# Kernel tuning notes

Hardware: AMD Instinct MI355X
Metric: run time of the kernel (lower is better)

## Reference

```python
import jax, jax.numpy as jnp
import numpy as np

N_PTS = 20000  # points per cloud


def setup_inputs() -> dict:
    key = jax.random.key(0)
    k1, k2 = jax.random.split(key)
    preds = jax.random.normal(k1, (N_PTS, 3), dtype=jnp.float32)
    gts = jax.random.normal(k2, (1, N_PTS, 3), dtype=jnp.float32)
    return {"preds": preds, "gts": gts}


def reference(preds, gts):
    # x = gts: [B, Nx, 3]; y = preds.unsqueeze(0): [1, Ny, 3] (B must be 1 for bmm)
    y = preds[None]                                   # [1, Ny, 3]
    x = gts                                           # [1, Nx, 3]
    xx = jnp.sum(x * x, axis=-1)                      # [1, Nx]  (diag of x x^T)
    yy = jnp.sum(y * y, axis=-1)                      # [1, Ny]
    zz = jnp.einsum('bnd,bmd->bnm', x, y)             # [1, Nx, Ny]
    P = xx[:, :, None] + yy[:, None, :] - 2.0 * zz    # [1, Nx, Ny] squared dists
    dist1 = jnp.min(P, axis=1)                        # [1, Ny] min over gts points
    dist2 = jnp.min(P, axis=2)                        # [1, Nx] min over pred points
    idx1 = jnp.argmin(P, axis=1)                      # [1, Ny]
    idx2 = jnp.argmin(P, axis=2)                      # [1, Nx]
    return dist1, dist2, idx1, idx2
```

## Files before the change

### kernel.cpp

```cpp
#include <hip/hip_runtime.h>

#define N_PTS  20000
#define NG     128
#define NC     (NG * NG)
#define GMIN   (-6.0f)
#define GINV   (NG / 12.0f)
#define MARGIN 5e-4f
#define SSTRIDE (N_PTS / 64)
#define QB79   79

__device__ __forceinline__ float np_self_dot(float x, float y, float z) {
    return __fadd_rn(__fadd_rn(__fmul_rn(x, x), __fmul_rn(y, y)),
                     __fmul_rn(z, z));
}
__device__ __forceinline__ unsigned ordmap(float f) {
    unsigned b = __float_as_uint(f);
    return (b & 0x80000000u) ? ~b : (b | 0x80000000u);
}
__device__ __forceinline__ float invord(unsigned h) {
    return __uint_as_float((h & 0x80000000u) ? (h ^ 0x80000000u) : ~h);
}
__device__ __forceinline__ int cellC(float v) {
    int c = (int)((v - GMIN) * GINV);
    return c < 0 ? 0 : (c > NG - 1 ? NG - 1 : c);
}
__device__ __forceinline__ unsigned long long wave_min_u64(unsigned long long k) {
    #pragma unroll
    for (int m = 1; m < 64; m <<= 1) {
        unsigned long long o = __shfl_xor(k, m, 64);
        k = (o < k) ? o : k;
    }
    return k;
}
__device__ __forceinline__ int imin2(int a, int b) { return a < b ? a : b; }
__device__ __forceinline__ int imax2(int a, int b) { return a > b ? a : b; }

#define EVAL2(r)                                                           \
    {   float rx = (r).x, ry = (r).y, rz = (r).z;                          \
        float sr = np_self_dot(rx, ry, rz);                                \
        unsigned ridx = __float_as_uint((r).w);                            \
        float za = __fadd_rn(__fadd_rn(__fmul_rn(qax, rx),                 \
                                       __fmul_rn(qay, ry)),                \
                             __fmul_rn(qaz, rz));                          \
        float Pa = __fsub_rn(__fadd_rn(sqa, sr), __fadd_rn(za, za));       \
        unsigned long long kka =                                           \
            ((unsigned long long)ordmap(Pa) << 32) | ridx;                 \
        ka = (kka < ka) ? kka : ka;                                        \
        float zb = __fadd_rn(__fadd_rn(__fmul_rn(qbx, rx),                 \
                                       __fmul_rn(qby, ry)),                \
                             __fmul_rn(qbz, rz));                          \
        float Pb = __fsub_rn(__fadd_rn(sqb, sr), __fadd_rn(zb, zb));       \
        unsigned long long kkb =                                           \
            ((unsigned long long)ordmap(Pb) << 32) | ridx;                 \
        kb = (kkb < kb) ? kkb : kb; }

__global__ __launch_bounds__(256) void k_hist(
    const float* __restrict__ preds, const float* __restrict__ gts,
    int* __restrict__ cursor)
{
    int t = blockIdx.x * 256 + threadIdx.x;
    if (t >= 2 * N_PTS) return;
    int cl = t / N_PTS, i = t - cl * N_PTS;
    const float* src = cl ? gts : preds;
    int cell = cellC(src[i*3+0]) * NG + cellC(src[i*3+1]);
    atomicAdd(&cursor[cl * NC + cell], 1);
}

__global__ __launch_bounds__(1024) void k_scan(
    int* __restrict__ cursor, int* __restrict__ bstart)
{
    __shared__ int wsum[16];
    __shared__ int wpre[16];
    int cl = blockIdx.x, t = threadIdx.x;
    int wave = t >> 6, lane = t & 63;

    int base = cl * NC + t * 16;
    const int4* c4 = (const int4*)(cursor + base);
    int4 a = c4[0], b = c4[1], c = c4[2], d = c4[3];
    int v[16] = { a.x, a.y, a.z, a.w, b.x, b.y, b.z, b.w,
                  c.x, c.y, c.z, c.w, d.x, d.y, d.z, d.w };
    int s = 0;
    #pragma unroll
    for (int i = 0; i < 16; ++i) s += v[i];

    int ps = s;
    #pragma unroll
    for (int m = 1; m < 64; m <<= 1) {
        int o = __shfl_up(ps, m, 64);
        if (lane >= m) ps += o;
    }
    if (lane == 63) wsum[wave] = ps;
    __syncthreads();
    if (t < 16) {
        int x = wsum[t];
        int px = x;
        #pragma unroll
        for (int m = 1; m < 16; m <<= 1) {
            int o = __shfl_up(px, m, 16);
            if ((t & 15) >= m) px += o;
        }
        wpre[t] = px - x;
    }
    __syncthreads();

    int run = wpre[wave] + (ps - s);
    #pragma unroll
    for (int i = 0; i < 16; ++i) {
        bstart[cl * (NC + 1) + t * 16 + i] = run;
        cursor[base + i] = run;
        run += v[i];
    }
    if (t == 1023) bstart[cl * (NC + 1) + NC] = run;
}

__global__ __launch_bounds__(256) void k_scatter(
    const float* __restrict__ preds, const float* __restrict__ gts,
    int* __restrict__ cursor, float4* __restrict__ sorted)
{
    int t = blockIdx.x * 256 + threadIdx.x;
    if (t >= 2 * N_PTS) return;
    int cl = t / N_PTS, i = t - cl * N_PTS;
    const float* src = cl ? gts : preds;
    float x = src[i*3+0], y = src[i*3+1], z = src[i*3+2];
    int cell = cellC(x) * NG + cellC(y);
    int pos = atomicAdd(&cursor[cl * NC + cell], 1);
    sorted[(size_t)cl * N_PTS + pos] = make_float4(x, y, z, __int_as_float(i));
}

__global__ __launch_bounds__(64) void k_main(
    const float4* __restrict__ sorted, const int* __restrict__ bstart,
    float* __restrict__ out)
{
    int wid  = blockIdx.x;
    int lane = threadIdx.x;
    int q0   = wid * 2;
    int dir  = q0 / N_PTS;
    int qp0  = q0 - dir * N_PTS;
    int rcl  = 1 - dir;

    const float4* rs = sorted + (size_t)rcl * N_PTS;
    const int*    cs = bstart + rcl * (NC + 1);

    float4 samp = rs[lane * SSTRIDE];
    float4 qva  = sorted[(size_t)dir * N_PTS + qp0];
    float4 qvb  = sorted[(size_t)dir * N_PTS + qp0 + 1];
    int oa = __float_as_int(qva.w), ob = __float_as_int(qvb.w);
    float qax = qva.x, qay = qva.y, qaz = qva.z;
    float qbx = qvb.x, qby = qvb.y, qbz = qvb.z;
    float sqa = np_self_dot(qax, qay, qaz);
    float sqb = np_self_dot(qbx, qby, qbz);

    unsigned long long ka = ~0ULL, kb = ~0ULL;
    int l31 = lane & 31;

#define SCAN_RECT(xL, xR, yL, yR)                                          \
    {   int R = (xR) - (xL) + 1;                                           \
        for (int g = 0; g < R; g += 32) {                                  \
            int rows = R - g; if (rows > 32) rows = 32;                    \
            int xr  = (xL) + g + (l31 < rows ? l31 : rows - 1);            \
            int col = (lane < 32) ? (yL) : ((yR) + 1);                     \
            int b2 = cs[xr * NG + col];                                    \
            for (int r0 = 0; r0 < rows; r0 += 3) {                         \
                int i1 = r0 + 1 < rows ? r0 + 1 : rows - 1;                \
                int i2 = r0 + 2 < rows ? r0 + 2 : rows - 1;                \
                int L0 = __shfl(b2, r0, 64), H0 = __shfl(b2, 32 + r0, 64); \
                int L1 = __shfl(b2, i1, 64), H1 = __shfl(b2, 32 + i1, 64); \
                int L2 = __shfl(b2, i2, 64), H2 = __shfl(b2, 32 + i2, 64); \
                int d0 = H0 - L0;                                          \
                int d1 = (r0 + 1 < rows) ? H1 - L1 : 0;                    \
                int d2 = (r0 + 2 < rows) ? H2 - L2 : 0;                    \
                int s01 = d0 + d1, tot = s01 + d2;                         \
                int t = lane;                                              \
                if (t < tot) {                                             \
                    int p = t < d0 ? L0 + t : t < s01 ? L1 + (t - d0)      \
                                                      : L2 + (t - s01);   \
                    float4 rc = rs[p];                                     \
                    for (t += 64; t < tot; t += 64) {                      \
                        int pn = t < d0 ? L0 + t : t < s01 ? L1 + (t - d0) \
                                                           : L2 + (t - s01);\
                        float4 rn = rs[pn];                                \
                        EVAL2(rc)                                          \
                        rc = rn;                                           \
                    }                                                      \
                    EVAL2(rc)                                              \
                }                                                          \
            }                                                              \
        }                                                                  \
    }

    int cxa = cellC(qax), cya = cellC(qay);
    int cxb = cellC(qbx), cyb = cellC(qby);
    int sxL = imax2(imin2(cxa, cxb) - 1, 0);
    int sxR = imin2(imax2(cxa, cxb) + 1, NG - 1);
    int syL = imax2(imin2(cya, cyb) - 1, 0);
    int syR = imin2(imax2(cya, cyb) + 1, NG - 1);
    SCAN_RECT(sxL, sxR, syL, syR)
    EVAL2(samp)

    ka = wave_min_u64(ka);
    kb = wave_min_u64(kb);
    float Wa = sqrtf(invord((unsigned)(ka >> 32)) + MARGIN);
    float Wb = sqrtf(invord((unsigned)(kb >> 32)) + MARGIN);
    int txL = imin2(cellC(qax - Wa), cellC(qbx - Wb));
    int txR = imax2(cellC(qax + Wa), cellC(qbx + Wb));
    int tyL = imin2(cellC(qay - Wa), cellC(qby - Wb));
    int tyR = imax2(cellC(qay + Wa), cellC(qby + Wb));
    if (!(txL >= sxL && txR <= sxR && tyL >= syL && tyR <= syR)) {
        SCAN_RECT(txL, txR, tyL, tyR)
        ka = wave_min_u64(ka);
        kb = wave_min_u64(kb);
    }
#undef SCAN_RECT

    if (lane == 0) {
        out[dir * N_PTS + oa]       = invord((unsigned)(ka >> 32));
        out[(2 + dir) * N_PTS + oa] = (float)(unsigned)(ka & 0xFFFFFFFFu);
        out[dir * N_PTS + ob]       = invord((unsigned)(kb >> 32));
        out[(2 + dir) * N_PTS + ob] = (float)(unsigned)(kb & 0xFFFFFFFFu);
    }
}

__device__ __forceinline__ float np_pair(float sq, float sr,
                                         float qx, float qy, float qz,
                                         float rx, float ry, float rz) {
    float zz = __fadd_rn(__fadd_rn(__fmul_rn(qx, rx), __fmul_rn(qy, ry)),
                         __fmul_rn(qz, rz));
    return __fsub_rn(__fadd_rn(sq, sr), __fadd_rn(zz, zz));
}

__global__ __launch_bounds__(256) void chamfer_direct_kernel(
    const float* __restrict__ preds, const float* __restrict__ gts,
    float* __restrict__ out)
{
    __shared__ float4 spts[256];
    int bid = blockIdx.x;
    int dir = bid / QB79;
    int qb  = bid - dir * QB79;
    int q   = qb * 256 + threadIdx.x;

    const float* qpts = (dir == 0) ? preds : gts;
    const float* rpts = (dir == 0) ? gts   : preds;

    int qc = (q < N_PTS) ? q : (N_PTS - 1);
    float qx = qpts[qc*3+0], qy = qpts[qc*3+1], qz = qpts[qc*3+2];
    float sq = np_self_dot(qx, qy, qz);
    float best = 3.4e38f;
    int   bidx = 0;

    for (int t = 0; t < N_PTS; t += 256) {
        int cnt = min(256, N_PTS - t);
        __syncthreads();
        if ((int)threadIdx.x < cnt) {
            int j = t + threadIdx.x;
            float rx = rpts[j*3+0], ry = rpts[j*3+1], rz = rpts[j*3+2];
            spts[threadIdx.x] = make_float4(rx, ry, rz, np_self_dot(rx, ry, rz));
        }
        __syncthreads();
        for (int k = 0; k < cnt; ++k) {
            float4 r = spts[k];
            float d = np_pair(sq, r.w, qx, qy, qz, r.x, r.y, r.z);
            if (d < best) { best = d; bidx = t + k; }
        }
    }
    if (q < N_PTS) {
        out[dir * N_PTS + q]       = best;
        out[(2 + dir) * N_PTS + q] = (float)bidx;
    }
}

extern "C" void kernel_launch(void* const* d_in, const int* in_sizes, int n_in,
                              void* d_out, int out_size, void* d_ws, size_t ws_size,
                              hipStream_t stream) {
    const float* preds = (const float*)d_in[0];
    const float* gts   = (const float*)d_in[1];
    float* out = (float*)d_out;

    char* w = (char*)d_ws;
    size_t sorted_b = (size_t)2 * N_PTS * sizeof(float4);
    size_t bstart_b = (size_t)2 * (NC + 1) * sizeof(int);
    size_t cursor_b = (size_t)2 * NC * sizeof(int);
    size_t need = sorted_b + bstart_b + cursor_b;

    if (ws_size >= need) {
        float4* sorted = (float4*)w;
        int* bstart = (int*)(w + sorted_b);
        int* cursor = (int*)(w + sorted_b + bstart_b);

        hipMemsetAsync(cursor, 0, cursor_b, stream);
        k_hist<<<(2 * N_PTS + 255) / 256, 256, 0, stream>>>(preds, gts, cursor);
        k_scan<<<2, 1024, 0, stream>>>(cursor, bstart);
        k_scatter<<<(2 * N_PTS + 255) / 256, 256, 0, stream>>>(
            preds, gts, cursor, sorted);
        k_main<<<N_PTS, 64, 0, stream>>>(sorted, bstart, out);
    } else {
        chamfer_direct_kernel<<<2 * QB79, 256, 0, stream>>>(preds, gts, out);
    }
}
```

Before: 135.8 us.

## Scan separate 5x5 cell neighborhoods per query instead of a shared bounding rectangle

Each wave previously handled two queries by scanning the union rectangle of both queries' 3x3 neighborhoods, and each candidate was evaluated against both queries. Now each query scans its own 5x5 cell window, evaluating only its own distance, and falls back to its own wider scan only if needed. This avoids wasted evaluations when the two queries are far apart and makes fallback rescans rarer, but when the queries are close it drops the shared loads and issues two serial scans with larger windows.

```diff
diff --git a/kernel.cpp b/kernel.cpp
--- a/kernel.cpp
+++ b/kernel.cpp
@@ -32,27 +32,54 @@
     }
     return k;
 }
-__device__ __forceinline__ int imin2(int a, int b) { return a < b ? a : b; }
-__device__ __forceinline__ int imax2(int a, int b) { return a > b ? a : b; }
-
-#define EVAL2(r)                                                           \
-    {   float rx = (r).x, ry = (r).y, rz = (r).z;                          \
-        float sr = np_self_dot(rx, ry, rz);                                \
-        unsigned ridx = __float_as_uint((r).w);                            \
-        float za = __fadd_rn(__fadd_rn(__fmul_rn(qax, rx),                 \
-                                       __fmul_rn(qay, ry)),                \
-                             __fmul_rn(qaz, rz));                          \
-        float Pa = __fsub_rn(__fadd_rn(sqa, sr), __fadd_rn(za, za));       \
-        unsigned long long kka =                                           \
-            ((unsigned long long)ordmap(Pa) << 32) | ridx;                 \
-        ka = (kka < ka) ? kka : ka;                                        \
-        float zb = __fadd_rn(__fadd_rn(__fmul_rn(qbx, rx),                 \
-                                       __fmul_rn(qby, ry)),                \
-                             __fmul_rn(qbz, rz));                          \
-        float Pb = __fsub_rn(__fadd_rn(sqb, sr), __fadd_rn(zb, zb));       \
-        unsigned long long kkb =                                           \
-            ((unsigned long long)ordmap(Pb) << 32) | ridx;                 \
-        kb = (kkb < kb) ? kkb : kb; }
+
+#define EVALQ(r, QX, QY, QZ, SQ, KEY)                                      \
+    {   float sr = np_self_dot((r).x, (r).y, (r).z);                       \
+        float zz = __fadd_rn(__fadd_rn(__fmul_rn(QX, (r).x),               \
+                                       __fmul_rn(QY, (r).y)),              \
+                             __fmul_rn(QZ, (r).z));                        \
+        float P  = __fsub_rn(__fadd_rn(SQ, sr), __fadd_rn(zz, zz));        \
+        unsigned long long kk =                                            \
+            ((unsigned long long)ordmap(P) << 32) | __float_as_uint((r).w);\
+        KEY = (kk < KEY) ? kk : KEY; }
+
+#define SCAN_ROWS32(BND, ROWS, QX, QY, QZ, SQ, KEY)                        \
+    for (int r0 = 0; r0 < (ROWS); r0 += 3) {                               \
+        int i1 = r0 + 1 < (ROWS) ? r0 + 1 : (ROWS) - 1;                    \
+        int i2 = r0 + 2 < (ROWS) ? r0 + 2 : (ROWS) - 1;                    \
+        int L0 = __shfl(BND, r0, 64), H0 = __shfl(BND, 32 + r0, 64);       \
+        int L1 = __shfl(BND, i1, 64), H1 = __shfl(BND, 32 + i1, 64);       \
+        int L2 = __shfl(BND, i2, 64), H2 = __shfl(BND, 32 + i2, 64);       \
+        int d0 = H0 - L0;                                                  \
+        int d1 = (r0 + 1 < (ROWS)) ? H1 - L1 : 0;                          \
+        int d2 = (r0 + 2 < (ROWS)) ? H2 - L2 : 0;                          \
+        int s01 = d0 + d1, tot = s01 + d2;                                 \
+        int t = lane;                                                      \
+        if (t < tot) {                                                     \
+            int p = t < d0 ? L0 + t : t < s01 ? L1 + (t - d0)              \
+                                              : L2 + (t - s01);            \
+            float4 rc = rs[p];                                             \
+            for (t += 64; t < tot; t += 64) {                              \
+                int pn = t < d0 ? L0 + t : t < s01 ? L1 + (t - d0)         \
+                                                   : L2 + (t - s01);       \
+                float4 rn = rs[pn];                                        \
+                EVALQ(rc, QX, QY, QZ, SQ, KEY)                             \
+                rc = rn;                                                   \
+            }                                                              \
+            EVALQ(rc, QX, QY, QZ, SQ, KEY)                                 \
+        }                                                                  \
+    }
+
+#define SCAN_RECT(xL, xR, yL, yR, QX, QY, QZ, SQ, KEY)                     \
+    {   int R = (xR) - (xL) + 1;                                           \
+        for (int g = 0; g < R; g += 32) {                                  \
+            int rows = R - g; if (rows > 32) rows = 32;                    \
+            int xr  = (xL) + g + (l31 < rows ? l31 : rows - 1);            \
+            int col = (lane < 32) ? (yL) : ((yR) + 1);                     \
+            int b2 = cs[xr * NG + col];                                    \
+            SCAN_ROWS32(b2, rows, QX, QY, QZ, SQ, KEY)                     \
+        }                                                                  \
+    }
 
 __global__ __launch_bounds__(256) void k_hist(
     const float* __restrict__ preds, const float* __restrict__ gts,
@@ -153,64 +180,42 @@
     unsigned long long ka = ~0ULL, kb = ~0ULL;
     int l31 = lane & 31;
 
-#define SCAN_RECT(xL, xR, yL, yR)                                          \
-    {   int R = (xR) - (xL) + 1;                                           \
-        for (int g = 0; g < R; g += 32) {                                  \
-            int rows = R - g; if (rows > 32) rows = 32;                    \
-            int xr  = (xL) + g + (l31 < rows ? l31 : rows - 1);            \
-            int col = (lane < 32) ? (yL) : ((yR) + 1);                     \
-            int b2 = cs[xr * NG + col];                                    \
-            for (int r0 = 0; r0 < rows; r0 += 3) {                         \
-                int i1 = r0 + 1 < rows ? r0 + 1 : rows - 1;                \
-                int i2 = r0 + 2 < rows ? r0 + 2 : rows - 1;                \
-                int L0 = __shfl(b2, r0, 64), H0 = __shfl(b2, 32 + r0, 64); \
-                int L1 = __shfl(b2, i1, 64), H1 = __shfl(b2, 32 + i1, 64); \
-                int L2 = __shfl(b2, i2, 64), H2 = __shfl(b2, 32 + i2, 64); \
-                int d0 = H0 - L0;                                          \
-                int d1 = (r0 + 1 < rows) ? H1 - L1 : 0;                    \
-                int d2 = (r0 + 2 < rows) ? H2 - L2 : 0;                    \
-                int s01 = d0 + d1, tot = s01 + d2;                         \
-                int t = lane;                                              \
-                if (t < tot) {                                             \
-                    int p = t < d0 ? L0 + t : t < s01 ? L1 + (t - d0)      \
-                                                      : L2 + (t - s01);   \
-                    float4 rc = rs[p];                                     \
-                    for (t += 64; t < tot; t += 64) {                      \
-                        int pn = t < d0 ? L0 + t : t < s01 ? L1 + (t - d0) \
-                                                           : L2 + (t - s01);\
-                        float4 rn = rs[pn];                                \
-                        EVAL2(rc)                                          \
-                        rc = rn;                                           \
-                    }                                                      \
-                    EVAL2(rc)                                              \
-                }                                                          \
-            }                                                              \
-        }                                                                  \
-    }
-
     int cxa = cellC(qax), cya = cellC(qay);
     int cxb = cellC(qbx), cyb = cellC(qby);
-    int sxL = imax2(imin2(cxa, cxb) - 1, 0);
-    int sxR = imin2(imax2(cxa, cxb) + 1, NG - 1);
-    int syL = imax2(imin2(cya, cyb) - 1, 0);
-    int syR = imin2(imax2(cya, cyb) + 1, NG - 1);
-    SCAN_RECT(sxL, sxR, syL, syR)
-    EVAL2(samp)
+    int sxLa = cxa > 1 ? cxa - 2 : 0, sxRa = cxa < NG-2 ? cxa + 2 : NG-1;
+    int syLa = cya > 1 ? cya - 2 : 0, syRa = cya < NG-2 ? cya + 2 : NG-1;
+    int sxLb = cxb > 1 ? cxb - 2 : 0, sxRb = cxb < NG-2 ? cxb + 2 : NG-1;
+    int syLb = cyb > 1 ? cyb - 2 : 0, syRb = cyb < NG-2 ? cyb + 2 : NG-1;
+    int nrsA = sxRa - sxLa + 1, nrsB = sxRb - sxLb + 1;
+    int xrA  = sxLa + (l31 < nrsA ? l31 : nrsA - 1);
+    int xrB  = sxLb + (l31 < nrsB ? l31 : nrsB - 1);
+    int colA = (lane < 32) ? syLa : (syRa + 1);
+    int colB = (lane < 32) ? syLb : (syRb + 1);
+    int bndA = cs[xrA * NG + colA];
+    int bndB = cs[xrB * NG + colB];
+
+    SCAN_ROWS32(bndA, nrsA, qax, qay, qaz, sqa, ka)
+    SCAN_ROWS32(bndB, nrsB, qbx, qby, qbz, sqb, kb)
+    EVALQ(samp, qax, qay, qaz, sqa, ka)
+    EVALQ(samp, qbx, qby, qbz, sqb, kb)
 
     ka = wave_min_u64(ka);
     kb = wave_min_u64(kb);
+
     float Wa = sqrtf(invord((unsigned)(ka >> 32)) + MARGIN);
     float Wb = sqrtf(invord((unsigned)(kb >> 32)) + MARGIN);
-    int txL = imin2(cellC(qax - Wa), cellC(qbx - Wb));
-    int txR = imax2(cellC(qax + Wa), cellC(qbx + Wb));
-    int tyL = imin2(cellC(qay - Wa), cellC(qby - Wb));
-    int tyR = imax2(cellC(qay + Wa), cellC(qby + Wb));
-    if (!(txL >= sxL && txR <= sxR && tyL >= syL && tyR <= syR)) {
-        SCAN_RECT(txL, txR, tyL, tyR)
+    int txLa = cellC(qax - Wa), txRa = cellC(qax + Wa);
+    int tyLa = cellC(qay - Wa), tyRa = cellC(qay + Wa);
+    int txLb = cellC(qbx - Wb), txRb = cellC(qbx + Wb);
+    int tyLb = cellC(qby - Wb), tyRb = cellC(qby + Wb);
+    if (!(txLa >= sxLa && txRa <= sxRa && tyLa >= syLa && tyRa <= syRa)) {
+        SCAN_RECT(txLa, txRa, tyLa, tyRa, qax, qay, qaz, sqa, ka)
         ka = wave_min_u64(ka);
+    }
+    if (!(txLb >= sxLb && txRb <= sxRb && tyLb >= syLb && tyRb <= syRb)) {
+        SCAN_RECT(txLb, txRb, tyLb, tyRb, qbx, qby, qbz, sqb, kb)
         kb = wave_min_u64(kb);
     }
-#undef SCAN_RECT
 
     if (lane == 0) {
         out[dir * N_PTS + oa]       = invord((unsigned)(ka >> 32));
```

Measured after the change: 118.7 us (median of 3 runs). 1.14x faster.
